# Kernel tuning notes

Hardware: AMD Instinct MI355X
Metric: run time of the kernel (lower is better)

The kernel has to match this reference:

```python
import jax, jax.numpy as jnp
import numpy as np

EPS = 1e-5

def _linear(x, w, b):
    # torch nn.Linear convention: w is [out, in]
    return jnp.einsum('...i,oi->...o', x, w) + b

def _l2_normalize(x, axis=-1):
    n = jnp.sqrt(jnp.sum(x * x, axis=axis, keepdims=True))
    return x / jnp.maximum(n, 1e-12)

def _online_softmax_scan(sim):
    # sim: [B, H, L]. Running max m_t and running sum s_t = sum_{i<=t} exp(sim_i - m_t)
    def combine(a, b):
        ma, sa = a
        mb, sb = b
        m = jnp.maximum(ma, mb)
        s = sa * jnp.exp(ma - m) + sb * jnp.exp(mb - m)
        return m, s
    m_scan, s_scan = jax.lax.associative_scan(combine, (sim, jnp.ones_like(sim)), axis=2)
    return m_scan, s_scan


def setup_inputs() -> dict:
    key = jax.random.key(0)
    ks = jax.random.split(key, 8)
    B, L, D = 2, 2048, 256
    H, h = 8, 32
    s = 1.0 / np.sqrt(D)
    inp = {
        'x': jax.random.normal(ks[0], (B, L, D), jnp.float32),
        'wq_w': jax.random.normal(ks[1], (D, D), jnp.float32) * s,
        'wq_b': jnp.zeros((D,), jnp.float32),
        'wk_w': jax.random.normal(ks[2], (D, D), jnp.float32) * s,
        'wk_b': jnp.zeros((D,), jnp.float32),
        'wv_w': jax.random.normal(ks[3], (D, D), jnp.float32) * s,
        'wv_b': jnp.zeros((D,), jnp.float32),
        'wo_w': jax.random.normal(ks[4], (D, D), jnp.float32) * s,
        'wo_b': jnp.zeros((D,), jnp.float32),
        'wg_w': jax.random.normal(ks[5], (1, h * h), jnp.float32) * (1.0 / np.sqrt(h * h)),
        'wg_b': jnp.zeros((1,), jnp.float32),
        'kv_norm_scale': jnp.ones((1, H, 1, h, h), jnp.float32),
        'qk_norm_scale': jnp.full((1, H, 1), 1.0 / np.sqrt(h), jnp.float32),
    }
    return inp


def reference(x, wq_w, wq_b, wk_w, wk_b, wv_w, wv_b, wo_w, wo_b,
              wg_w, wg_b, kv_norm_scale, qk_norm_scale):
    B, L, D = x.shape
    H, h = kv_norm_scale.shape[1], kv_norm_scale.shape[3]

    q = _linear(x, wq_w, wq_b).reshape(B, L, H, h).transpose(0, 2, 1, 3)  # bhld
    k = _linear(x, wk_w, wk_b).reshape(B, L, H, h).transpose(0, 2, 1, 3)
    v = _linear(x, wv_w, wv_b).reshape(B, L, H, h).transpose(0, 2, 1, 3)

    sim = jnp.einsum('bhld,bhld->bhl', q, k) * qk_norm_scale  # [B,H,L]

    k = _l2_normalize(k)
    v = _l2_normalize(v)

    # outer-product KV state per position: [B,H,L,h,h]
    Z = jnp.einsum('bhld,bhle->bhlde', v, k) * kv_norm_scale

    # gating: squared ReLU of linear over flattened h*h features
    gate_inputs = Z.reshape(B, H, L, h * h)
    gates_logits = jnp.einsum('bhli,oi->bhlo', gate_inputs, wg_w) + wg_b  # [B,H,L,1]
    gates = jnp.square(jax.nn.relu(gates_logits)) + EPS
    gates = gates[..., None]  # [B,H,L,1,1]
    gated_Z = gates * Z

    # associative scans along L
    m_scan, s_scan = _online_softmax_scan(sim)        # [B,H,L]
    Z_scan = jnp.cumsum(gated_Z, axis=2)              # [B,H,L,h,h]
    g_scan = jnp.cumsum(gates, axis=2)                # [B,H,L,1,1]

    softmax_weights = (jnp.exp(sim - m_scan) / (s_scan + EPS))[..., None, None]
    gated_weights = Z_scan / (g_scan + EPS)
    attn_weights = gated_weights * (1.0 + jax.nn.silu(softmax_weights))

    ctxt = jnp.einsum('bhld,bhlde->bhle', q, attn_weights)
    ctxt = ctxt.transpose(0, 2, 1, 3).reshape(B, L, D)
    return _linear(ctxt, wo_w, wo_b)
```

## Files before the change

kernel.cpp:

```cpp
#include <hip/hip_runtime.h>
#include <math.h>

#define EPSV 1e-5f

static constexpr int Ls = 2048, Hh = 8;
static constexpr int NCH = 64, T = 32;

typedef unsigned short u16;
using frag  = __attribute__((ext_vector_type(8))) short;
using f32x4 = __attribute__((ext_vector_type(4))) float;

__device__ __forceinline__ void split_bf16(float v, u16& hi, u16& lo) {
    const unsigned u = __float_as_uint(v);
    hi = (u16)(u >> 16);
    const float hf = __uint_as_float((unsigned)hi << 16);
    lo = (u16)(__float_as_uint(v - hf) >> 16);
}

__global__ __launch_bounds__(256) void convert_kernel(
    const float* __restrict__ x, const float* __restrict__ wq,
    const float* __restrict__ wk, const float* __restrict__ wv,
    const float* __restrict__ wo,
    u16* __restrict__ xhi, u16* __restrict__ xlo,
    u16* __restrict__ whi, u16* __restrict__ wlo)
{
    const int gi = blockIdx.x * 256 + threadIdx.x;
    const float* src;
    u16 *dhi, *dlo;
    size_t off;
    if (gi < 262144) {
        src = x; off = gi; dhi = xhi; dlo = xlo;
    } else {
        const int t = gi - 262144;
        const int w = t >> 14, o = t & 16383;
        src = w == 0 ? wq : w == 1 ? wk : w == 2 ? wv : wo;
        off = o;
        dhi = whi + (size_t)w * 65536;
        dlo = wlo + (size_t)w * 65536;
    }
    const float4 v = ((const float4*)src)[off];
    ushort4 h, l;
    split_bf16(v.x, h.x, l.x);
    split_bf16(v.y, h.y, l.y);
    split_bf16(v.z, h.z, l.z);
    split_bf16(v.w, h.w, l.w);
    ((ushort4*)dhi)[off] = h;
    ((ushort4*)dlo)[off] = l;
}

__global__ __launch_bounds__(256) void mfma_gemm(
    const u16* __restrict__ Ahi, const u16* __restrict__ Alo,
    const u16* __restrict__ Whi_all, const u16* __restrict__ Wlo_all,
    const float* __restrict__ bq, const float* __restrict__ bk, const float* __restrict__ bv,
    float* __restrict__ oq, float* __restrict__ ok_, float* __restrict__ ov,
    int mode)
{
    constexpr int LDK = 40;
    __shared__ u16 As_hi[128 * LDK], As_lo[128 * LDK];
    __shared__ u16 Bs_hi[64 * LDK],  Bs_lo[64 * LDK];

    const int tid = threadIdx.x;
    const int mt = blockIdx.x, nt = blockIdx.y;
    int ncol0, which;
    const float* bp;
    float* Op;
    if (mode == 0) {
        which = nt >> 2;
        ncol0 = (nt & 3) * 64;
        bp = which == 0 ? bq : which == 1 ? bk : bv;
        Op = which == 0 ? oq : which == 1 ? ok_ : ov;
    } else {
        which = 3;
        ncol0 = nt * 64;
        bp = bq;
        Op = oq;
    }
    const u16* Whi = Whi_all + (size_t)which * 65536;
    const u16* Wlo = Wlo_all + (size_t)which * 65536;

    const int m0 = mt * 128;
    const int srow = tid >> 2, skc = tid & 3;
    const int wave = tid >> 6, lane = tid & 63;
    const int l15 = lane & 15, quad = lane >> 4;
    const int wm0 = (wave >> 1) * 64, wn0 = (wave & 1) * 32;

    f32x4 acc[4][2] = {};

    for (int k0 = 0; k0 < 256; k0 += 32) {
        const size_t ga0 = (size_t)(m0 + srow) * 256 + k0 + skc * 8;
        const size_t ga1 = (size_t)(m0 + 64 + srow) * 256 + k0 + skc * 8;
        const size_t gb  = (size_t)(ncol0 + srow) * 256 + k0 + skc * 8;
        const uint4 ah0 = *(const uint4*)&Ahi[ga0];
        const uint4 ah1 = *(const uint4*)&Ahi[ga1];
        const uint4 al0 = *(const uint4*)&Alo[ga0];
        const uint4 al1 = *(const uint4*)&Alo[ga1];
        const uint4 bh0 = *(const uint4*)&Whi[gb];
        const uint4 bl0 = *(const uint4*)&Wlo[gb];
        __syncthreads();
        *(uint4*)&As_hi[srow * LDK + skc * 8] = ah0;
        *(uint4*)&As_hi[(64 + srow) * LDK + skc * 8] = ah1;
        *(uint4*)&As_lo[srow * LDK + skc * 8] = al0;
        *(uint4*)&As_lo[(64 + srow) * LDK + skc * 8] = al1;
        *(uint4*)&Bs_hi[srow * LDK + skc * 8] = bh0;
        *(uint4*)&Bs_lo[srow * LDK + skc * 8] = bl0;
        __syncthreads();

        frag ah[4], al[4], bh[2], bl[2];
#pragma unroll
        for (int tm = 0; tm < 4; ++tm) {
            const int r = wm0 + tm * 16 + l15;
            ah[tm] = *(const frag*)&As_hi[r * LDK + quad * 8];
            al[tm] = *(const frag*)&As_lo[r * LDK + quad * 8];
        }
#pragma unroll
        for (int tn = 0; tn < 2; ++tn) {
            const int r = wn0 + tn * 16 + l15;
            bh[tn] = *(const frag*)&Bs_hi[r * LDK + quad * 8];
            bl[tn] = *(const frag*)&Bs_lo[r * LDK + quad * 8];
        }
#pragma unroll
        for (int tm = 0; tm < 4; ++tm)
#pragma unroll
            for (int tn = 0; tn < 2; ++tn) {
                acc[tm][tn] = __builtin_amdgcn_mfma_f32_16x16x32_bf16(ah[tm], bh[tn], acc[tm][tn], 0, 0, 0);
                acc[tm][tn] = __builtin_amdgcn_mfma_f32_16x16x32_bf16(ah[tm], bl[tn], acc[tm][tn], 0, 0, 0);
                acc[tm][tn] = __builtin_amdgcn_mfma_f32_16x16x32_bf16(al[tm], bh[tn], acc[tm][tn], 0, 0, 0);
            }
    }

#pragma unroll
    for (int tn = 0; tn < 2; ++tn) {
        const int o = ncol0 + wn0 + tn * 16 + l15;
        const float bias = bp[o];
        const int hd = o >> 5, e = o & 31;
#pragma unroll
        for (int tm = 0; tm < 4; ++tm)
#pragma unroll
            for (int r = 0; r < 4; ++r) {
                const int rm = m0 + wm0 + tm * 16 + quad * 4 + r;
                const float val = acc[tm][tn][r] + bias;
                if (mode == 0) {
                    const int b = rm >> 11, l = rm & (Ls - 1);
                    Op[(((size_t)(b * Hh + hd)) * Ls + l) * 32 + e] = val;
                } else {
                    Op[(size_t)rm * 256 + o] = val;
                }
            }
    }
}

__global__ __launch_bounds__(1024) void chunk_sum_kernel(
    const float* __restrict__ qh, float* __restrict__ kh, float* __restrict__ vh,
    const float* __restrict__ wg_w, const float* __restrict__ wg_b,
    const float* __restrict__ kvs, const float* __restrict__ qks,
    float* __restrict__ simG, float* __restrict__ gG,
    float* __restrict__ ZcT, float* __restrict__ mT, float* __restrict__ sT,
    float* __restrict__ gTt)
{
    __shared__ float lkn[1024], lvn[1024], lwk[1024], lsim[T], lg[T];
    const int tid = threadIdx.x;
    const int c = blockIdx.x, bh = blockIdx.y, h = bh & 7;
    const int l = tid >> 5, lane = tid & 31;
    const size_t base = ((size_t)bh * Ls + c * T) * 32;

    const float qv = qh[base + tid];
    const float kv = kh[base + tid];
    const float vv = vh[base + tid];
    lwk[tid] = wg_w[tid] * kvs[h * 1024 + tid];

    float qk = qv * kv, ks = kv * kv, vs = vv * vv;
#pragma unroll
    for (int off = 16; off; off >>= 1) {
        qk += __shfl_xor(qk, off);
        ks += __shfl_xor(ks, off);
        vs += __shfl_xor(vs, off);
    }
    const float kn = kv / fmaxf(sqrtf(ks), 1e-12f);
    const float vn = vv / fmaxf(sqrtf(vs), 1e-12f);
    kh[base + tid] = kn;
    vh[base + tid] = vn;
    lkn[tid] = kn;
    lvn[tid] = vn;
    if (lane == 0) {
        const float s = qk * qks[h];
        lsim[l] = s;
        simG[bh * Ls + c * T + l] = s;
    }
    __syncthreads();

    float t = 0.f;
#pragma unroll 8
    for (int d = 0; d < 32; ++d)
        t = fmaf(lvn[l * 32 + d], lwk[d * 32 + lane], t);
    t *= lkn[l * 32 + lane];
#pragma unroll
    for (int off = 16; off; off >>= 1) t += __shfl_xor(t, off);
    if (lane == 0) {
        const float r = fmaxf(t + wg_b[0], 0.f);
        const float g = r * r + EPSV;
        lg[l] = g;
        gG[bh * Ls + c * T + l] = g;
    }
    __syncthreads();

    {
        const int e = tid & 31, d = tid >> 5;
        float z = 0.f;
#pragma unroll 8
        for (int l2 = 0; l2 < T; ++l2)
            z = fmaf(lg[l2] * lvn[l2 * 32 + d], lkn[l2 * 32 + e], z);
        ZcT[((size_t)bh * NCH + c) * 1024 + tid] = z;
    }

    if (tid < 32) {
        float m = lsim[tid], s = 1.f, g = lg[tid];
#pragma unroll
        for (int off = 16; off; off >>= 1) {
            const float mo = __shfl_xor(m, off);
            const float so = __shfl_xor(s, off);
            const float mn = fmaxf(m, mo);
            s = s * __expf(m - mn) + so * __expf(mo - mn);
            m = mn;
            g += __shfl_xor(g, off);
        }
        if (tid == 0) {
            mT[bh * NCH + c] = m;
            sT[bh * NCH + c] = s;
            gTt[bh * NCH + c] = g;
        }
    }
}

__global__ __launch_bounds__(256) void prefix_kernel(
    float* __restrict__ Zc, float* __restrict__ mT, float* __restrict__ sT,
    float* __restrict__ gTt,
    const float* __restrict__ kvs, float* __restrict__ aW, float* __restrict__ bW,
    int* __restrict__ flagW)
{
    const int bh = blockIdx.x, seg = blockIdx.y;
    const int tid = threadIdx.x;
    const int el = seg * 256 + tid;
    float* Zb = Zc + (size_t)bh * NCH * 1024 + el;

    float run = 0.f;
#pragma unroll
    for (int cb = 0; cb < NCH; cb += 8) {
        float v[8];
#pragma unroll
        for (int i = 0; i < 8; ++i) v[i] = Zb[(size_t)(cb + i) * 1024];
#pragma unroll
        for (int i = 0; i < 8; ++i) {
            const float t = v[i];
            Zb[(size_t)(cb + i) * 1024] = run;
            run += t;
        }
    }

    if (seg == 0 && tid < 64) {
        float m = mT[bh * NCH + tid], s = sT[bh * NCH + tid], g = gTt[bh * NCH + tid];
#pragma unroll
        for (int off = 1; off < 64; off <<= 1) {
            const float mo = __shfl_up(m, off);
            const float so = __shfl_up(s, off);
            const float go = __shfl_up(g, off);
            if (tid >= off) {
                const float mn = fmaxf(m, mo);
                s = s * __expf(m - mn) + so * __expf(mo - mn);
                m = mn;
                g += go;
            }
        }
        float me = __shfl_up(m, 1), se = __shfl_up(s, 1), ge = __shfl_up(g, 1);
        if (tid == 0) { me = -1e30f; se = 0.f; ge = 0.f; }
        mT[bh * NCH + tid] = me;
        sT[bh * NCH + tid] = se;
        gTt[bh * NCH + tid] = ge;
    }

    if (bh == 0 && seg == 3) {
        const int h = tid >> 5, e = tid & 31;
        const float* K = kvs + h * 1024;
        const float k00 = K[0];
        int ok = (k00 != 0.0f);
        for (int d = 0; d < 32; ++d) {
            const float lhs = K[d * 32 + e] * k00;
            const float rhs = K[d * 32] * K[e];
            const float diff = fabsf(lhs - rhs);
            if (diff > 1e-6f * fmaxf(fmaxf(fabsf(lhs), fabsf(rhs)), 1e-20f)) ok = 0;
        }
        aW[h * 32 + e] = K[e * 32];
        bW[h * 32 + e] = (k00 != 0.0f) ? K[e] / k00 : 0.f;
        const int allok = __syncthreads_and(ok);
        if (tid == 0) flagW[0] = allok;
    }
}

__global__ __launch_bounds__(1024) void chunk_out_kernel(
    const float* __restrict__ qh, const float* __restrict__ knG, const float* __restrict__ vnG,
    const float* __restrict__ simG, const float* __restrict__ gG,
    const float* __restrict__ kvs,
    const float* __restrict__ ZcP, const float* __restrict__ mP,
    const float* __restrict__ sP, const float* __restrict__ gP,
    const float* __restrict__ aW, const float* __restrict__ bW,
    const int* __restrict__ flagW,
    u16* __restrict__ chi, u16* __restrict__ clo)
{
    __shared__ float qa[1024], knb[1024], zp[1024], lkvs[1024];
    __shared__ float vnT[32 * 33], sW[32 * 33];
    __shared__ float la[32], lb[32], lg[T], lsim[T], lwgt[T];
    const int tid = threadIdx.x;
    const int c = blockIdx.x, bh = blockIdx.y, h = bh & 7, b = bh >> 3;
    const int l = tid >> 5, lane = tid & 31;
    const size_t base = ((size_t)bh * Ls + c * T) * 32;
    const int flag = flagW[0];

    const float qv = qh[base + tid];
    const float knv = knG[base + tid];
    const float vnv = vnG[base + tid];
    vnT[lane * 33 + l] = vnv;
    zp[tid] = ZcP[((size_t)bh * NCH + c) * 1024 + tid];
    if (!flag) lkvs[tid] = kvs[h * 1024 + tid];
    if (tid < 32) {
        la[tid] = aW[h * 32 + tid];
        lb[tid] = bW[h * 32 + tid];
        lg[tid] = gG[bh * Ls + c * T + tid];
        lsim[tid] = simG[bh * Ls + c * T + tid];
    }
    __syncthreads();

    qa[tid] = flag ? qv * la[lane] : qv;
    knb[tid] = flag ? knv * lb[lane] : knv;
    if (tid < 32) {
        float m = lsim[tid], s = 1.f, g = lg[tid];
#pragma unroll
        for (int off = 1; off < 32; off <<= 1) {
            const float mo = __shfl_up(m, off);
            const float so = __shfl_up(s, off);
            const float go = __shfl_up(g, off);
            if (tid >= off) {
                const float mn = fmaxf(m, mo);
                s = s * __expf(m - mn) + so * __expf(mo - mn);
                m = mn;
                g += go;
            }
        }
        const float mp = mP[bh * NCH + c];
        const float sp = sP[bh * NCH + c];
        const float gp = gP[bh * NCH + c];
        const float mn = fmaxf(mp, m);
        s = sp * __expf(mp - mn) + s * __expf(m - mn);
        m = mn;
        g += gp;
        const float sw = __expf(lsim[tid] - m) / (s + EPSV);
        const float sig = 1.f / (1.f + __expf(-sw));
        lwgt[tid] = (1.f + sw * sig) / (g + EPSV);
    }
    __syncthreads();

    float y;
    if (flag) {
        float s = 0.f, y0 = 0.f;
        const float4* qa4 = (const float4*)&qa[l * 32];
#pragma unroll
        for (int d4 = 0; d4 < 8; ++d4) {
            const float4 q4 = qa4[d4];
            const int d = d4 * 4;
            s = fmaf(q4.x, vnT[(d + 0) * 33 + lane], s);
            s = fmaf(q4.y, vnT[(d + 1) * 33 + lane], s);
            s = fmaf(q4.z, vnT[(d + 2) * 33 + lane], s);
            s = fmaf(q4.w, vnT[(d + 3) * 33 + lane], s);
            y0 = fmaf(q4.x, zp[(d + 0) * 32 + lane], y0);
            y0 = fmaf(q4.y, zp[(d + 1) * 32 + lane], y0);
            y0 = fmaf(q4.z, zp[(d + 2) * 32 + lane], y0);
            y0 = fmaf(q4.w, zp[(d + 3) * 32 + lane], y0);
        }
        sW[l * 33 + lane] = (lane <= l) ? lg[lane] * s : 0.f;
        __syncthreads();
        y = y0 * lb[lane];
#pragma unroll 8
        for (int j = 0; j < 32; ++j)
            y = fmaf(sW[l * 33 + j], knb[j * 32 + lane], y);
        y *= lwgt[l];
    } else {
        float qe[32];
#pragma unroll
        for (int d = 0; d < 32; ++d)
            qe[d] = qa[l * 32 + d] * lkvs[d * 32 + lane];
        y = 0.f;
#pragma unroll
        for (int d = 0; d < 32; ++d)
            y = fmaf(qe[d], zp[d * 32 + lane], y);
        for (int j = 0; j < 32; ++j) {
            float s = 0.f;
#pragma unroll
            for (int d = 0; d < 32; ++d)
                s = fmaf(qe[d], vnT[d * 33 + j], s);
            if (j <= l) y = fmaf(lg[j] * s, knb[j * 32 + lane], y);
        }
        y *= lwgt[l];
    }
    u16 hi, lo;
    split_bf16(y, hi, lo);
    const size_t oidx = ((size_t)(b * Ls + c * T + l)) * 256 + h * 32 + lane;
    chi[oidx] = hi;
    clo[oidx] = lo;
}

extern "C" void kernel_launch(void* const* d_in, const int* in_sizes, int n_in,
                              void* d_out, int out_size, void* d_ws, size_t ws_size,
                              hipStream_t stream) {
    const float* x    = (const float*)d_in[0];
    const float* wq_w = (const float*)d_in[1];
    const float* wq_b = (const float*)d_in[2];
    const float* wk_w = (const float*)d_in[3];
    const float* wk_b = (const float*)d_in[4];
    const float* wv_w = (const float*)d_in[5];
    const float* wv_b = (const float*)d_in[6];
    const float* wo_w = (const float*)d_in[7];
    const float* wo_b = (const float*)d_in[8];
    const float* wg_w = (const float*)d_in[9];
    const float* wg_b = (const float*)d_in[10];
    const float* kvs  = (const float*)d_in[11];
    const float* qks  = (const float*)d_in[12];
    float* out = (float*)d_out;

    u16* xhi = (u16*)d_ws;
    u16* xlo = xhi + 1048576;
    u16* whi = xlo + 1048576;
    u16* wlo = whi + 262144;
    u16* chi = wlo + 262144;
    u16* clo = chi + 1048576;
    float* qh   = (float*)(clo + 1048576);
    float* kh   = qh + 1048576;
    float* vh   = kh + 1048576;
    float* ZcT  = vh + 1048576;
    float* simG = ZcT + 1048576;
    float* gG   = simG + 32768;
    float* mT   = gG + 32768;
    float* sT   = mT + 1024;
    float* gTt  = sT + 1024;
    float* aW   = gTt + 1024;
    float* bW   = aW + 256;
    int* flagW  = (int*)(bW + 256);

    convert_kernel<<<1280, 256, 0, stream>>>(
        x, wq_w, wk_w, wv_w, wo_w, xhi, xlo, whi, wlo);
    mfma_gemm<<<dim3(32, 12), 256, 0, stream>>>(
        xhi, xlo, whi, wlo, wq_b, wk_b, wv_b, qh, kh, vh, 0);
    chunk_sum_kernel<<<dim3(NCH, 16), 1024, 0, stream>>>(
        qh, kh, vh, wg_w, wg_b, kvs, qks, simG, gG, ZcT, mT, sT, gTt);
    prefix_kernel<<<dim3(16, 4), 256, 0, stream>>>(
        ZcT, mT, sT, gTt, kvs, aW, bW, flagW);
    chunk_out_kernel<<<dim3(NCH, 16), 1024, 0, stream>>>(
        qh, kh, vh, simG, gG, kvs, ZcT, mT, sT, gTt, aW, bW, flagW, chi, clo);
    mfma_gemm<<<dim3(32, 4), 256, 0, stream>>>(
        chi, clo, whi, wlo, wo_b, nullptr, nullptr, out, nullptr, nullptr, 1);
}
```

Measured before the change: 147.3 us.

## Fuse bf16 split, QKV GEMM and chunk summaries into one kernel

New measurement: 145.2 us. No clear change (-1.4%).

```diff
diff --git a/kernel.cpp b/kernel.cpp
--- a/kernel.cpp
+++ b/kernel.cpp
@@ -17,216 +17,232 @@
     lo = (u16)(__float_as_uint(v - hf) >> 16);
 }
 
-__global__ __launch_bounds__(256) void convert_kernel(
-    const float* __restrict__ x, const float* __restrict__ wq,
-    const float* __restrict__ wk, const float* __restrict__ wv,
-    const float* __restrict__ wo,
-    u16* __restrict__ xhi, u16* __restrict__ xlo,
-    u16* __restrict__ whi, u16* __restrict__ wlo)
-{
-    const int gi = blockIdx.x * 256 + threadIdx.x;
-    const float* src;
-    u16 *dhi, *dlo;
-    size_t off;
-    if (gi < 262144) {
-        src = x; off = gi; dhi = xhi; dlo = xlo;
-    } else {
-        const int t = gi - 262144;
-        const int w = t >> 14, o = t & 16383;
-        src = w == 0 ? wq : w == 1 ? wk : w == 2 ? wv : wo;
-        off = o;
-        dhi = whi + (size_t)w * 65536;
-        dlo = wlo + (size_t)w * 65536;
-    }
-    const float4 v = ((const float4*)src)[off];
-    ushort4 h, l;
-    split_bf16(v.x, h.x, l.x);
-    split_bf16(v.y, h.y, l.y);
-    split_bf16(v.z, h.z, l.z);
-    split_bf16(v.w, h.w, l.w);
-    ((ushort4*)dhi)[off] = h;
-    ((ushort4*)dlo)[off] = l;
-}
-
-__global__ __launch_bounds__(256) void mfma_gemm(
-    const u16* __restrict__ Ahi, const u16* __restrict__ Alo,
-    const u16* __restrict__ Whi_all, const u16* __restrict__ Wlo_all,
+__device__ __forceinline__ unsigned pk2(u16 a, u16 b) {
+    return (unsigned)a | ((unsigned)b << 16);
+}
+
+__device__ __forceinline__ void split8(const float4& a, const float4& b,
+                                       uint4& hi, uint4& lo) {
+    u16 h[8], l[8];
+    const float f[8] = {a.x, a.y, a.z, a.w, b.x, b.y, b.z, b.w};
+#pragma unroll
+    for (int i = 0; i < 8; ++i) split_bf16(f[i], h[i], l[i]);
+    hi = make_uint4(pk2(h[0], h[1]), pk2(h[2], h[3]), pk2(h[4], h[5]), pk2(h[6], h[7]));
+    lo = make_uint4(pk2(l[0], l[1]), pk2(l[2], l[3]), pk2(l[4], l[5]), pk2(l[6], l[7]));
+}
+
+__global__ __launch_bounds__(256) void qkv_fused(
+    const float* __restrict__ x,
+    const float* __restrict__ wq, const float* __restrict__ wk, const float* __restrict__ wv,
     const float* __restrict__ bq, const float* __restrict__ bk, const float* __restrict__ bv,
-    float* __restrict__ oq, float* __restrict__ ok_, float* __restrict__ ov,
-    int mode)
-{
-    constexpr int LDK = 40;
-    __shared__ u16 As_hi[128 * LDK], As_lo[128 * LDK];
-    __shared__ u16 Bs_hi[64 * LDK],  Bs_lo[64 * LDK];
-
-    const int tid = threadIdx.x;
-    const int mt = blockIdx.x, nt = blockIdx.y;
-    int ncol0, which;
-    const float* bp;
-    float* Op;
-    if (mode == 0) {
-        which = nt >> 2;
-        ncol0 = (nt & 3) * 64;
-        bp = which == 0 ? bq : which == 1 ? bk : bv;
-        Op = which == 0 ? oq : which == 1 ? ok_ : ov;
-    } else {
-        which = 3;
-        ncol0 = nt * 64;
-        bp = bq;
-        Op = oq;
-    }
-    const u16* Whi = Whi_all + (size_t)which * 65536;
-    const u16* Wlo = Wlo_all + (size_t)which * 65536;
-
-    const int m0 = mt * 128;
-    const int srow = tid >> 2, skc = tid & 3;
-    const int wave = tid >> 6, lane = tid & 63;
-    const int l15 = lane & 15, quad = lane >> 4;
-    const int wm0 = (wave >> 1) * 64, wn0 = (wave & 1) * 32;
-
-    f32x4 acc[4][2] = {};
-
-    for (int k0 = 0; k0 < 256; k0 += 32) {
-        const size_t ga0 = (size_t)(m0 + srow) * 256 + k0 + skc * 8;
-        const size_t ga1 = (size_t)(m0 + 64 + srow) * 256 + k0 + skc * 8;
-        const size_t gb  = (size_t)(ncol0 + srow) * 256 + k0 + skc * 8;
-        const uint4 ah0 = *(const uint4*)&Ahi[ga0];
-        const uint4 ah1 = *(const uint4*)&Ahi[ga1];
-        const uint4 al0 = *(const uint4*)&Alo[ga0];
-        const uint4 al1 = *(const uint4*)&Alo[ga1];
-        const uint4 bh0 = *(const uint4*)&Whi[gb];
-        const uint4 bl0 = *(const uint4*)&Wlo[gb];
-        __syncthreads();
-        *(uint4*)&As_hi[srow * LDK + skc * 8] = ah0;
-        *(uint4*)&As_hi[(64 + srow) * LDK + skc * 8] = ah1;
-        *(uint4*)&As_lo[srow * LDK + skc * 8] = al0;
-        *(uint4*)&As_lo[(64 + srow) * LDK + skc * 8] = al1;
-        *(uint4*)&Bs_hi[srow * LDK + skc * 8] = bh0;
-        *(uint4*)&Bs_lo[srow * LDK + skc * 8] = bl0;
-        __syncthreads();
-
-        frag ah[4], al[4], bh[2], bl[2];
-#pragma unroll
-        for (int tm = 0; tm < 4; ++tm) {
-            const int r = wm0 + tm * 16 + l15;
-            ah[tm] = *(const frag*)&As_hi[r * LDK + quad * 8];
-            al[tm] = *(const frag*)&As_lo[r * LDK + quad * 8];
-        }
-#pragma unroll
-        for (int tn = 0; tn < 2; ++tn) {
-            const int r = wn0 + tn * 16 + l15;
-            bh[tn] = *(const frag*)&Bs_hi[r * LDK + quad * 8];
-            bl[tn] = *(const frag*)&Bs_lo[r * LDK + quad * 8];
-        }
-#pragma unroll
-        for (int tm = 0; tm < 4; ++tm)
-#pragma unroll
-            for (int tn = 0; tn < 2; ++tn) {
-                acc[tm][tn] = __builtin_amdgcn_mfma_f32_16x16x32_bf16(ah[tm], bh[tn], acc[tm][tn], 0, 0, 0);
-                acc[tm][tn] = __builtin_amdgcn_mfma_f32_16x16x32_bf16(ah[tm], bl[tn], acc[tm][tn], 0, 0, 0);
-                acc[tm][tn] = __builtin_amdgcn_mfma_f32_16x16x32_bf16(al[tm], bh[tn], acc[tm][tn], 0, 0, 0);
-            }
-    }
-
-#pragma unroll
-    for (int tn = 0; tn < 2; ++tn) {
-        const int o = ncol0 + wn0 + tn * 16 + l15;
-        const float bias = bp[o];
-        const int hd = o >> 5, e = o & 31;
-#pragma unroll
-        for (int tm = 0; tm < 4; ++tm)
-#pragma unroll
-            for (int r = 0; r < 4; ++r) {
-                const int rm = m0 + wm0 + tm * 16 + quad * 4 + r;
-                const float val = acc[tm][tn][r] + bias;
-                if (mode == 0) {
-                    const int b = rm >> 11, l = rm & (Ls - 1);
-                    Op[(((size_t)(b * Hh + hd)) * Ls + l) * 32 + e] = val;
-                } else {
-                    Op[(size_t)rm * 256 + o] = val;
-                }
-            }
-    }
-}
-
-__global__ __launch_bounds__(1024) void chunk_sum_kernel(
-    const float* __restrict__ qh, float* __restrict__ kh, float* __restrict__ vh,
     const float* __restrict__ wg_w, const float* __restrict__ wg_b,
     const float* __restrict__ kvs, const float* __restrict__ qks,
+    float* __restrict__ qh, float* __restrict__ kh, float* __restrict__ vh,
     float* __restrict__ simG, float* __restrict__ gG,
     float* __restrict__ ZcT, float* __restrict__ mT, float* __restrict__ sT,
     float* __restrict__ gTt)
 {
-    __shared__ float lkn[1024], lvn[1024], lwk[1024], lsim[T], lg[T];
+    constexpr int LDK = 40;
+    constexpr int LDT = 66;
+    __shared__ __align__(16) float smemf[3 * 64 * LDT];
+    __shared__ float wkS[2][1024];
+    __shared__ float lsim[2][64], lg2[2][64];
+
+    u16* As_hi = (u16*)smemf;
+    u16* As_lo = As_hi + 2560;
+    u16* Wst   = As_lo + 2560;
+    float* Qt = smemf;
+    float* Kt = Qt + 64 * LDT;
+    float* Vt = Kt + 64 * LDT;
+
     const int tid = threadIdx.x;
-    const int c = blockIdx.x, bh = blockIdx.y, h = bh & 7;
-    const int l = tid >> 5, lane = tid & 31;
-    const size_t base = ((size_t)bh * Ls + c * T) * 32;
-
-    const float qv = qh[base + tid];
-    const float kv = kh[base + tid];
-    const float vv = vh[base + tid];
-    lwk[tid] = wg_w[tid] * kvs[h * 1024 + tid];
-
-    float qk = qv * kv, ks = kv * kv, vs = vv * vv;
-#pragma unroll
-    for (int off = 16; off; off >>= 1) {
-        qk += __shfl_xor(qk, off);
-        ks += __shfl_xor(ks, off);
-        vs += __shfl_xor(vs, off);
-    }
-    const float kn = kv / fmaxf(sqrtf(ks), 1e-12f);
-    const float vn = vv / fmaxf(sqrtf(vs), 1e-12f);
-    kh[base + tid] = kn;
-    vh[base + tid] = vn;
-    lkn[tid] = kn;
-    lvn[tid] = vn;
-    if (lane == 0) {
-        const float s = qk * qks[h];
-        lsim[l] = s;
-        simG[bh * Ls + c * T + l] = s;
+    const int mt = blockIdx.x, nt = blockIdx.y;
+    const int m0 = mt * 64, ncol0 = nt * 64;
+    const int bidx = m0 >> 11, lg = m0 & (Ls - 1);
+    const int wave = tid >> 6, lane = tid & 63;
+    const int l15 = lane & 15, quad = lane >> 4;
+    const int srow = tid >> 2, sk = (tid & 3) * 8;
+
+    for (int i = tid; i < 2048; i += 256) {
+        const int h = i >> 10, de = i & 1023;
+        wkS[h][de] = wg_w[de] * kvs[(nt * 2 + h) * 1024 + de];
+    }
+
+    const float* Wsrc[3] = {wq, wk, wv};
+    f32x4 acc[3][4] = {};
+
+    for (int k0 = 0; k0 < 256; k0 += 32) {
+        const float4 a0 = *(const float4*)&x[(size_t)(m0 + srow) * 256 + k0 + sk];
+        const float4 a1 = *(const float4*)&x[(size_t)(m0 + srow) * 256 + k0 + sk + 4];
+        float4 w0[3], w1[3];
+#pragma unroll
+        for (int w = 0; w < 3; ++w) {
+            w0[w] = *(const float4*)&Wsrc[w][(size_t)(ncol0 + srow) * 256 + k0 + sk];
+            w1[w] = *(const float4*)&Wsrc[w][(size_t)(ncol0 + srow) * 256 + k0 + sk + 4];
+        }
+        __syncthreads();
+        {
+            uint4 hi, lo;
+            split8(a0, a1, hi, lo);
+            *(uint4*)&As_hi[srow * LDK + sk] = hi;
+            *(uint4*)&As_lo[srow * LDK + sk] = lo;
+#pragma unroll
+            for (int w = 0; w < 3; ++w) {
+                split8(w0[w], w1[w], hi, lo);
+                *(uint4*)&Wst[w * 5120 + srow * LDK + sk] = hi;
+                *(uint4*)&Wst[w * 5120 + 2560 + srow * LDK + sk] = lo;
+            }
+        }
+        __syncthreads();
+
+        const frag ah = *(const frag*)&As_hi[(wave * 16 + l15) * LDK + quad * 8];
+        const frag al = *(const frag*)&As_lo[(wave * 16 + l15) * LDK + quad * 8];
+#pragma unroll
+        for (int w = 0; w < 3; ++w)
+#pragma unroll
+            for (int cf = 0; cf < 4; ++cf) {
+                const u16* bp = &Wst[w * 5120 + (cf * 16 + l15) * LDK + quad * 8];
+                const frag bh = *(const frag*)bp;
+                const frag bl = *(const frag*)(bp + 2560);
+                acc[w][cf] = __builtin_amdgcn_mfma_f32_16x16x32_bf16(ah, bh, acc[w][cf], 0, 0, 0);
+                acc[w][cf] = __builtin_amdgcn_mfma_f32_16x16x32_bf16(ah, bl, acc[w][cf], 0, 0, 0);
+                acc[w][cf] = __builtin_amdgcn_mfma_f32_16x16x32_bf16(al, bh, acc[w][cf], 0, 0, 0);
+            }
     }
     __syncthreads();
 
-    float t = 0.f;
+    {
+        float* tiles[3] = {Qt, Kt, Vt};
+        const float* biases[3] = {bq, bk, bv};
+#pragma unroll
+        for (int w = 0; w < 3; ++w)
+#pragma unroll
+            for (int cf = 0; cf < 4; ++cf) {
+                const int col = cf * 16 + l15;
+                const float bias = biases[w][ncol0 + col];
+#pragma unroll
+                for (int r = 0; r < 4; ++r) {
+                    const int m = wave * 16 + quad * 4 + r;
+                    tiles[w][m * LDT + col] = acc[w][cf][r] + bias;
+                }
+            }
+    }
+    __syncthreads();
+
+    if (tid < 128) {
+        const int h = tid >> 6, l = tid & 63;
+        const int cb = h * 32;
+        float ksum = 0.f, vsum = 0.f, qk = 0.f;
 #pragma unroll 8
-    for (int d = 0; d < 32; ++d)
-        t = fmaf(lvn[l * 32 + d], lwk[d * 32 + lane], t);
-    t *= lkn[l * 32 + lane];
-#pragma unroll
-    for (int off = 16; off; off >>= 1) t += __shfl_xor(t, off);
-    if (lane == 0) {
-        const float r = fmaxf(t + wg_b[0], 0.f);
-        const float g = r * r + EPSV;
-        lg[l] = g;
-        gG[bh * Ls + c * T + l] = g;
+        for (int e = 0; e < 32; ++e) {
+            const float kv = Kt[l * LDT + cb + e];
+            const float vv = Vt[l * LDT + cb + e];
+            const float qv = Qt[l * LDT + cb + e];
+            ksum = fmaf(kv, kv, ksum);
+            vsum = fmaf(vv, vv, vsum);
+            qk = fmaf(qv, kv, qk);
+        }
+        const float kscale = 1.f / fmaxf(sqrtf(ksum), 1e-12f);
+        const float vscale = 1.f / fmaxf(sqrtf(vsum), 1e-12f);
+#pragma unroll 8
+        for (int e = 0; e < 32; ++e) {
+            Kt[l * LDT + cb + e] *= kscale;
+            Vt[l * LDT + cb + e] *= vscale;
+        }
+        const float sim = qk * qks[nt * 2 + h];
+        lsim[h][l] = sim;
+        simG[(size_t)(bidx * 8 + nt * 2 + h) * Ls + lg + l] = sim;
     }
     __syncthreads();
 
     {
-        const int e = tid & 31, d = tid >> 5;
-        float z = 0.f;
+        const float* tl[3] = {Qt, Kt, Vt};
+        float* gl[3] = {qh, kh, vh};
+#pragma unroll
+        for (int arr = 0; arr < 3; ++arr)
+#pragma unroll
+            for (int it = 0; it < 8; ++it) {
+                const int idx = it * 512 + tid * 2;
+                const int h = idx >> 11, rem = idx & 2047;
+                const int l = rem >> 5, e = rem & 31;
+                float2 v;
+                v.x = tl[arr][l * LDT + h * 32 + e];
+                v.y = tl[arr][l * LDT + h * 32 + e + 1];
+                *(float2*)&gl[arr][(size_t)(bidx * 8 + nt * 2 + h) * 65536 +
+                                   (size_t)(lg + l) * 32 + e] = v;
+            }
+    }
+
+    {
+        const int task = tid >> 1, half = tid & 1;
+        const int h = task >> 6, l = task & 63;
+        float vreg[32];
 #pragma unroll 8
-        for (int l2 = 0; l2 < T; ++l2)
-            z = fmaf(lg[l2] * lvn[l2 * 32 + d], lkn[l2 * 32 + e], z);
-        ZcT[((size_t)bh * NCH + c) * 1024 + tid] = z;
-    }
-
-    if (tid < 32) {
-        float m = lsim[tid], s = 1.f, g = lg[tid];
-#pragma unroll
-        for (int off = 16; off; off >>= 1) {
-            const float mo = __shfl_xor(m, off);
-            const float so = __shfl_xor(s, off);
-            const float mn = fmaxf(m, mo);
-            s = s * __expf(m - mn) + so * __expf(mo - mn);
-            m = mn;
-            g += __shfl_xor(g, off);
-        }
-        if (tid == 0) {
-            mT[bh * NCH + c] = m;
-            sT[bh * NCH + c] = s;
-            gTt[bh * NCH + c] = g;
+        for (int d = 0; d < 32; ++d) vreg[d] = Vt[l * LDT + h * 32 + d];
+        float u = 0.f;
+        const int e0 = half * 16;
+#pragma unroll 4
+        for (int e = e0; e < e0 + 16; ++e) {
+            float s = 0.f;
+#pragma unroll 8
+            for (int d = 0; d < 32; ++d)
+                s = fmaf(vreg[d], wkS[h][d * 32 + e], s);
+            u = fmaf(s, Kt[l * LDT + h * 32 + e], u);
+        }
+        u += __shfl_xor(u, 1);
+        if (half == 0) {
+            const float r = fmaxf(u + wg_b[0], 0.f);
+            const float g = r * r + EPSV;
+            lg2[h][l] = g;
+            gG[(size_t)(bidx * 8 + nt * 2 + h) * Ls + lg + l] = g;
+        }
+    }
+    __syncthreads();
+
+    {
+        const int d = tid >> 3, e0 = (tid & 7) * 4;
+#pragma unroll
+        for (int h = 0; h < 2; ++h)
+#pragma unroll
+            for (int cc = 0; cc < 2; ++cc) {
+                float z0 = 0.f, z1 = 0.f, z2 = 0.f, z3 = 0.f;
+#pragma unroll 8
+                for (int l = 0; l < 32; ++l) {
+                    const int lr = cc * 32 + l;
+                    const float gv = lg2[h][lr] * Vt[lr * LDT + h * 32 + d];
+                    z0 = fmaf(gv, Kt[lr * LDT + h * 32 + e0 + 0], z0);
+                    z1 = fmaf(gv, Kt[lr * LDT + h * 32 + e0 + 1], z1);
+                    z2 = fmaf(gv, Kt[lr * LDT + h * 32 + e0 + 2], z2);
+                    z3 = fmaf(gv, Kt[lr * LDT + h * 32 + e0 + 3], z3);
+                }
+                const int bhg = bidx * 8 + nt * 2 + h;
+                const int cg = (lg >> 5) + cc;
+                float4 zv; zv.x = z0; zv.y = z1; zv.z = z2; zv.w = z3;
+                *(float4*)&ZcT[((size_t)bhg * NCH + cg) * 1024 + d * 32 + e0] = zv;
+            }
+    }
+
+    {
+        const int h = wave >> 1, cc = wave & 1;
+        if (lane < 32) {
+            const int lr = cc * 32 + lane;
+            float m = lsim[h][lr], s = 1.f, g = lg2[h][lr];
+#pragma unroll
+            for (int off = 16; off; off >>= 1) {
+                const float mo = __shfl_xor(m, off);
+                const float so = __shfl_xor(s, off);
+                const float mn = fmaxf(m, mo);
+                s = s * __expf(m - mn) + so * __expf(mo - mn);
+                m = mn;
+                g += __shfl_xor(g, off);
+            }
+            if (lane == 0) {
+                const int bhg = bidx * 8 + nt * 2 + h;
+                const int cg = (lg >> 5) + cc;
+                mT[bhg * NCH + cg] = m;
+                sT[bhg * NCH + cg] = s;
+                gTt[bhg * NCH + cg] = g;
+            }
         }
     }
 }
@@ -406,6 +422,64 @@
     clo[oidx] = lo;
 }
 
+__global__ __launch_bounds__(256) void out_gemm(
+    const u16* __restrict__ Ahi, const u16* __restrict__ Alo,
+    const float* __restrict__ wo, const float* __restrict__ bo,
+    float* __restrict__ out)
+{
+    constexpr int LDK = 40;
+    __shared__ __align__(16) u16 As_hi[64 * LDK];
+    __shared__ __align__(16) u16 As_lo[64 * LDK];
+    __shared__ __align__(16) u16 Ws_hi[64 * LDK];
+    __shared__ __align__(16) u16 Ws_lo[64 * LDK];
+
+    const int tid = threadIdx.x;
+    const int mt = blockIdx.x, nt = blockIdx.y;
+    const int m0 = mt * 64, ncol0 = nt * 64;
+    const int wave = tid >> 6, lane = tid & 63;
+    const int l15 = lane & 15, quad = lane >> 4;
+    const int srow = tid >> 2, sk = (tid & 3) * 8;
+
+    f32x4 acc[4] = {};
+
+    for (int k0 = 0; k0 < 256; k0 += 32) {
+        const uint4 ah = *(const uint4*)&Ahi[(size_t)(m0 + srow) * 256 + k0 + sk];
+        const uint4 al = *(const uint4*)&Alo[(size_t)(m0 + srow) * 256 + k0 + sk];
+        const float4 w0 = *(const float4*)&wo[(size_t)(ncol0 + srow) * 256 + k0 + sk];
+        const float4 w1 = *(const float4*)&wo[(size_t)(ncol0 + srow) * 256 + k0 + sk + 4];
+        __syncthreads();
+        uint4 whi, wlo;
+        split8(w0, w1, whi, wlo);
+        *(uint4*)&As_hi[srow * LDK + sk] = ah;
+        *(uint4*)&As_lo[srow * LDK + sk] = al;
+        *(uint4*)&Ws_hi[srow * LDK + sk] = whi;
+        *(uint4*)&Ws_lo[srow * LDK + sk] = wlo;
+        __syncthreads();
+
+        const frag fah = *(const frag*)&As_hi[(wave * 16 + l15) * LDK + quad * 8];
+        const frag fal = *(const frag*)&As_lo[(wave * 16 + l15) * LDK + quad * 8];
+#pragma unroll
+        for (int cf = 0; cf < 4; ++cf) {
+            const frag fbh = *(const frag*)&Ws_hi[(cf * 16 + l15) * LDK + quad * 8];
+            const frag fbl = *(const frag*)&Ws_lo[(cf * 16 + l15) * LDK + quad * 8];
+            acc[cf] = __builtin_amdgcn_mfma_f32_16x16x32_bf16(fah, fbh, acc[cf], 0, 0, 0);
+            acc[cf] = __builtin_amdgcn_mfma_f32_16x16x32_bf16(fah, fbl, acc[cf], 0, 0, 0);
+            acc[cf] = __builtin_amdgcn_mfma_f32_16x16x32_bf16(fal, fbh, acc[cf], 0, 0, 0);
+        }
+    }
+
+#pragma unroll
+    for (int cf = 0; cf < 4; ++cf) {
+        const int o = ncol0 + cf * 16 + l15;
+        const float bias = bo[o];
+#pragma unroll
+        for (int r = 0; r < 4; ++r) {
+            const int rm = m0 + wave * 16 + quad * 4 + r;
+            out[(size_t)rm * 256 + o] = acc[cf][r] + bias;
+        }
+    }
+}
+
 extern "C" void kernel_launch(void* const* d_in, const int* in_sizes, int n_in,
                               void* d_out, int out_size, void* d_ws, size_t ws_size,
                               hipStream_t stream) {
@@ -424,11 +498,7 @@
     const float* qks  = (const float*)d_in[12];
     float* out = (float*)d_out;
 
-    u16* xhi = (u16*)d_ws;
-    u16* xlo = xhi + 1048576;
-    u16* whi = xlo + 1048576;
-    u16* wlo = whi + 262144;
-    u16* chi = wlo + 262144;
+    u16* chi = (u16*)d_ws;
     u16* clo = chi + 1048576;
     float* qh   = (float*)(clo + 1048576);
     float* kh   = qh + 1048576;
@@ -443,16 +513,13 @@
     float* bW   = aW + 256;
     int* flagW  = (int*)(bW + 256);
 
-    convert_kernel<<<1280, 256, 0, stream>>>(
-        x, wq_w, wk_w, wv_w, wo_w, xhi, xlo, whi, wlo);
-    mfma_gemm<<<dim3(32, 12), 256, 0, stream>>>(
-        xhi, xlo, whi, wlo, wq_b, wk_b, wv_b, qh, kh, vh, 0);
-    chunk_sum_kernel<<<dim3(NCH, 16), 1024, 0, stream>>>(
-        qh, kh, vh, wg_w, wg_b, kvs, qks, simG, gG, ZcT, mT, sT, gTt);
+    qkv_fused<<<dim3(64, 4), 256, 0, stream>>>(
+        x, wq_w, wk_w, wv_w, wq_b, wk_b, wv_b, wg_w, wg_b, kvs, qks,
+        qh, kh, vh, simG, gG, ZcT, mT, sT, gTt);
     prefix_kernel<<<dim3(16, 4), 256, 0, stream>>>(
         ZcT, mT, sT, gTt, kvs, aW, bW, flagW);
     chunk_out_kernel<<<dim3(NCH, 16), 1024, 0, stream>>>(
         qh, kh, vh, simG, gG, kvs, ZcT, mT, sT, gTt, aW, bW, flagW, chi, clo);
-    mfma_gemm<<<dim3(32, 4), 256, 0, stream>>>(
-        chi, clo, whi, wlo, wo_b, nullptr, nullptr, out, nullptr, nullptr, 1);
-}
+    out_gemm<<<dim3(64, 4), 256, 0, stream>>>(
+        chi, clo, wo_w, wo_b, out);
+}
```
